# Kernel optimization log

Measured on AMD Instinct MI355X. Metric: run time of the kernel, lower is better.

## Reference

```python
import jax, jax.numpy as jnp
import numpy as np

B, IN_DIM, OUT_DIM, DEPTH = 8192, 4096, 2048, 9


def setup_inputs() -> dict:
    key = jax.random.key(0)
    k1, k2, k3, k4 = jax.random.split(key, 4)
    return {
        "x": jax.random.normal(k1, (B, IN_DIM), dtype=jnp.float32),
        "universal_weights": jax.random.normal(k2, (DEPTH, IN_DIM, OUT_DIM), dtype=jnp.float32),
        "classical_weights": jax.random.normal(k3, (IN_DIM, OUT_DIM), dtype=jnp.float32),
        "classical_biases": jax.random.normal(k4, (OUT_DIM,), dtype=jnp.float32),
    }


def _universal_probs(universal_weights, out_dim, in_dim):
    # Angles: original indexes universal_weights[depth, j, c] with j over output
    # dims and c in {0,1,2} (consciousness/intelligence/wisdom gates per depth).
    # Build the scan sequence in (depth, gate) order: shape (3*DEPTH, O).
    A = jnp.transpose(universal_weights[:, :out_dim, :3], (0, 2, 1)).reshape(-1, out_dim)
    # Initial state ones/sqrt(n), one independent state per output channel: (O, n)
    s0 = jnp.full((out_dim, in_dim), 1.0 / np.sqrt(in_dim), dtype=universal_weights.dtype)

    def step(s, ang):
        # Circulant tridiagonal rotation: diag=cos, super(+wrap)=-sin, sub(+wrap)=sin
        c = jnp.cos(ang)[:, None]
        sn = jnp.sin(ang)[:, None]
        s_next = c * s - sn * jnp.roll(s, -1, axis=1) + sn * jnp.roll(s, 1, axis=1)
        return s_next, None

    s, _ = jax.lax.scan(step, s0, A)
    # probability = |state[0]|^2 ; state is real so this is just the square
    return s[:, 0] ** 2  # (O,)


def reference(x, universal_weights, classical_weights, classical_biases):
    out_dim = classical_weights.shape[1]
    in_dim = x.shape[1]
    classical = x @ classical_weights + classical_biases  # (B, O)
    # Universal output is independent of the batch row (loop over i is dead code)
    probs = _universal_probs(universal_weights, out_dim, in_dim)  # (O,)
    return jnp.tanh(classical + probs[None, :])
```

## Files before the change

### kernel.cpp

```cpp
#include <hip/hip_runtime.h>
#include <cstdint>
#include <cstddef>

#define MM 8192
#define KK 4096
#define NN 2048
#define DEPTH_N 9

typedef __attribute__((ext_vector_type(8))) short bf16x8;
typedef __attribute__((ext_vector_type(16))) float f32x16;

static_assert(sizeof(bf16x8) == 16, "bf16x8 must be 16B");
static_assert(sizeof(f32x16) == 64, "f32x16 must be 64B");

typedef const __attribute__((address_space(1))) uint32_t* gptr_t;
typedef __attribute__((address_space(3))) uint32_t* lptr_t;

__device__ __forceinline__ void load_lds16(const void* g, void* l) {
  __builtin_amdgcn_global_load_lds((gptr_t)g, (lptr_t)l, 16, 0, 0);
}

union FragU {
  uint32_t u[4];
  bf16x8 v;
};

__device__ __forceinline__ void split4(float4 v, uint32_t& h01, uint32_t& h23,
                                       uint32_t& l01, uint32_t& l23) {
  uint32_t ux = __float_as_uint(v.x), uy = __float_as_uint(v.y);
  uint32_t uz = __float_as_uint(v.z), uw = __float_as_uint(v.w);
  h01 = __builtin_amdgcn_perm(uy, ux, 0x07060302u);
  h23 = __builtin_amdgcn_perm(uw, uz, 0x07060302u);
  float rx = v.x - __uint_as_float(ux & 0xFFFF0000u);
  float ry = v.y - __uint_as_float(uy & 0xFFFF0000u);
  float rz = v.z - __uint_as_float(uz & 0xFFFF0000u);
  float rw = v.w - __uint_as_float(uw & 0xFFFF0000u);
  l01 = __builtin_amdgcn_perm(__float_as_uint(ry), __float_as_uint(rx), 0x07060302u);
  l23 = __builtin_amdgcn_perm(__float_as_uint(rw), __float_as_uint(rz), 0x07060302u);
}

__global__ __launch_bounds__(256) void prep_bt_kernel(
    const float* __restrict__ W,
    uint16_t* __restrict__ btHi,
    uint16_t* __restrict__ btLo) {
  __shared__ float tile[64][65];
  const int k0 = blockIdx.x * 64;
  const int n0 = blockIdx.y * 64;
  const int c4 = (threadIdx.x & 15) * 4;
  const int r16 = threadIdx.x >> 4;
#pragma unroll
  for (int p = 0; p < 4; ++p) {
    int r = p * 16 + r16;
    float4 v = *(const float4*)(W + (size_t)(k0 + r) * NN + n0 + c4);
    tile[r][c4 + 0] = v.x;
    tile[r][c4 + 1] = v.y;
    tile[r][c4 + 2] = v.z;
    tile[r][c4 + 3] = v.w;
  }
  __syncthreads();
#pragma unroll
  for (int p = 0; p < 4; ++p) {
    int n = p * 16 + r16;
    ushort4 h, l;
    float f0 = tile[c4 + 0][n];
    float f1 = tile[c4 + 1][n];
    float f2 = tile[c4 + 2][n];
    float f3 = tile[c4 + 3][n];
    uint32_t u0 = __float_as_uint(f0), u1 = __float_as_uint(f1);
    uint32_t u2 = __float_as_uint(f2), u3 = __float_as_uint(f3);
    h.x = (uint16_t)(u0 >> 16);
    h.y = (uint16_t)(u1 >> 16);
    h.z = (uint16_t)(u2 >> 16);
    h.w = (uint16_t)(u3 >> 16);
    float r0 = f0 - __uint_as_float(u0 & 0xFFFF0000u);
    float r1 = f1 - __uint_as_float(u1 & 0xFFFF0000u);
    float r2 = f2 - __uint_as_float(u2 & 0xFFFF0000u);
    float r3 = f3 - __uint_as_float(u3 & 0xFFFF0000u);
    l.x = (uint16_t)(__float_as_uint(r0) >> 16);
    l.y = (uint16_t)(__float_as_uint(r1) >> 16);
    l.z = (uint16_t)(__float_as_uint(r2) >> 16);
    l.w = (uint16_t)(__float_as_uint(r3) >> 16);
    size_t off = (size_t)(n0 + n) * KK + k0 + c4;
    *(ushort4*)(btHi + off) = h;
    *(ushort4*)(btLo + off) = l;
  }
}

__global__ __launch_bounds__(256) void prep_x_kernel(
    const float* __restrict__ X,
    uint16_t* __restrict__ xHi,
    uint16_t* __restrict__ xLo) {
  size_t i = ((size_t)blockIdx.x * 256 + threadIdx.x) * 8;
  float4 v0 = *(const float4*)(X + i);
  float4 v1 = *(const float4*)(X + i + 4);
  uint32_t h01, h23, l01, l23, h45, h67, l45, l67;
  split4(v0, h01, h23, l01, l23);
  split4(v1, h45, h67, l45, l67);
  uint4 h, l;
  h.x = h01; h.y = h23; h.z = h45; h.w = h67;
  l.x = l01; l.y = l23; l.z = l45; l.w = l67;
  *(uint4*)(xHi + i) = h;
  *(uint4*)(xLo + i) = l;
}

__global__ __launch_bounds__(256) void prep_bias_kernel(
    const float* __restrict__ uw,
    const float* __restrict__ cb,
    float* __restrict__ bias2) {
  int j = blockIdx.x * 256 + threadIdx.x;
  float p = 1.0f / (float)KK;
#pragma unroll
  for (int d = 0; d < DEPTH_N; ++d) {
    float4 v = *(const float4*)(uw + (size_t)d * KK * NN + (size_t)j * NN);
    float c0 = cosf(v.x), c1 = cosf(v.y), c2 = cosf(v.z);
    p *= (c0 * c0) * (c1 * c1) * (c2 * c2);
  }
  bias2[j] = cb[j] + p;
}

__global__ __launch_bounds__(256, 4) void unl_gemm_ps_kernel(
    const uint16_t* __restrict__ XHi,
    const uint16_t* __restrict__ XLo,
    const uint16_t* __restrict__ BtHi,
    const uint16_t* __restrict__ BtLo,
    const float* __restrict__ bias2,
    float* __restrict__ Out) {
  __shared__ __align__(16) uint8_t smem[32768];
  char* sAh = (char*)smem;
  char* sAl = (char*)smem + 8192;
  char* sBh = (char*)smem + 16384;
  char* sBl = (char*)smem + 24576;

  const int tid = threadIdx.x;
  const int lane = tid & 63;
  const int wq = __builtin_amdgcn_readfirstlane(tid >> 6);
  const int wM = wq >> 1;
  const int wN = wq & 1;
  const int lane31 = lane & 31;
  const int kh = lane >> 5;

  const int bidx = blockIdx.x;
  const int m0 = (bidx & 63) * 128;
  const int n0 = (bidx >> 6) * 128;

  const int bC = (lane & 3) ^ ((lane >> 3) & 3);
  const int bVoff = ((lane >> 2) * KK + bC * 8) * 2;
  const char* aBaseH = (const char*)(XHi + (size_t)(m0 + wq * 32) * KK) + bVoff;
  const char* aBaseL = (const char*)(XLo + (size_t)(m0 + wq * 32) * KK) + bVoff;
  const char* bBaseH = (const char*)(BtHi + (size_t)(n0 + wq * 32) * KK) + bVoff;
  const char* bBaseL = (const char*)(BtLo + (size_t)(n0 + wq * 32) * KK) + bVoff;

  int aOffB[2][2], bOffB[2][2];
#pragma unroll
  for (int mt = 0; mt < 2; ++mt) {
    int row = wM * 64 + mt * 32 + lane31;
#pragma unroll
    for (int s = 0; s < 2; ++s)
      aOffB[mt][s] = row * 64 + (((2 * s + kh) ^ ((row >> 1) & 3)) * 16);
  }
#pragma unroll
  for (int nt = 0; nt < 2; ++nt) {
    int row = wN * 64 + nt * 32 + lane31;
#pragma unroll
    for (int s = 0; s < 2; ++s)
      bOffB[nt][s] = row * 64 + (((2 * s + kh) ^ ((row >> 1) & 3)) * 16);
  }

  f32x16 acc[2][2];
#pragma unroll
  for (int mt = 0; mt < 2; ++mt)
#pragma unroll
    for (int nt = 0; nt < 2; ++nt)
#pragma unroll
      for (int r = 0; r < 16; ++r) acc[mt][nt][r] = 0.0f;

  for (int kt = 0; kt < KK; kt += 32) {
    __syncthreads();
#pragma unroll
    for (int q = 0; q < 2; ++q) {
      load_lds16(aBaseH + (size_t)kt * 2 + (size_t)q * (16 * KK * 2),
                 sAh + (wq * 2 + q) * 1024);
      load_lds16(aBaseL + (size_t)kt * 2 + (size_t)q * (16 * KK * 2),
                 sAl + (wq * 2 + q) * 1024);
      load_lds16(bBaseH + (size_t)kt * 2 + (size_t)q * (16 * KK * 2),
                 sBh + (wq * 2 + q) * 1024);
      load_lds16(bBaseL + (size_t)kt * 2 + (size_t)q * (16 * KK * 2),
                 sBl + (wq * 2 + q) * 1024);
    }
    __syncthreads();

#pragma unroll
    for (int s = 0; s < 2; ++s) {
      bf16x8 ah[2], al[2], bh[2], bl[2];
#pragma unroll
      for (int mt = 0; mt < 2; ++mt) {
        ah[mt] = *(const bf16x8*)(sAh + aOffB[mt][s]);
        al[mt] = *(const bf16x8*)(sAl + aOffB[mt][s]);
      }
#pragma unroll
      for (int nt = 0; nt < 2; ++nt) {
        bh[nt] = *(const bf16x8*)(sBh + bOffB[nt][s]);
        bl[nt] = *(const bf16x8*)(sBl + bOffB[nt][s]);
      }
#pragma unroll
      for (int mt = 0; mt < 2; ++mt) {
#pragma unroll
        for (int nt = 0; nt < 2; ++nt) {
          acc[mt][nt] = __builtin_amdgcn_mfma_f32_32x32x16_bf16(ah[mt], bh[nt], acc[mt][nt], 0, 0, 0);
          acc[mt][nt] = __builtin_amdgcn_mfma_f32_32x32x16_bf16(ah[mt], bl[nt], acc[mt][nt], 0, 0, 0);
          acc[mt][nt] = __builtin_amdgcn_mfma_f32_32x32x16_bf16(al[mt], bh[nt], acc[mt][nt], 0, 0, 0);
        }
      }
    }
  }

#pragma unroll
  for (int nt = 0; nt < 2; ++nt) {
    int col = n0 + wN * 64 + nt * 32 + lane31;
    float b2 = bias2[col];
#pragma unroll
    for (int mt = 0; mt < 2; ++mt) {
#pragma unroll
      for (int r = 0; r < 16; ++r) {
        int rowl = (r & 3) + 8 * (r >> 2) + 4 * kh;
        int grow = m0 + wM * 64 + mt * 32 + rowl;
        float z = acc[mt][nt][r] + b2;
        z = fminf(fmaxf(z, -12.0f), 12.0f);
        float t = __expf(2.0f * z);
        Out[(size_t)grow * NN + col] = (t - 1.0f) / (t + 1.0f);
      }
    }
  }
}

__global__ __launch_bounds__(256, 4) void unl_gemm_kernel(
    const float* __restrict__ X,
    const uint16_t* __restrict__ BtHi,
    const uint16_t* __restrict__ BtLo,
    const float* __restrict__ bias2,
    float* __restrict__ Out) {
  __shared__ __align__(16) uint8_t smem[32768];
  char* sA = (char*)smem;
  char* sBh = (char*)smem + 16384;
  char* sBl = (char*)smem + 24576;

  const int tid = threadIdx.x;
  const int lane = tid & 63;
  const int wq = __builtin_amdgcn_readfirstlane(tid >> 6);
  const int wM = wq >> 1;
  const int wN = wq & 1;
  const int lane31 = lane & 31;
  const int kh = lane >> 5;

  const int bidx = blockIdx.x;
  const int m0 = (bidx & 63) * 128;
  const int n0 = (bidx >> 6) * 128;

  const int aC = (lane & 7) ^ (lane >> 3);
  const int aVoff = ((lane >> 3) * KK + aC * 4) * 4;
  const char* aBase = (const char*)(X + (size_t)(m0 + wq * 32) * KK) + aVoff;
  const int bC = (lane & 3) ^ ((lane >> 3) & 3);
  const int bVoff = ((lane >> 2) * KK + bC * 8) * 2;
  const char* bBaseH = (const char*)(BtHi + (size_t)(n0 + wq * 32) * KK) + bVoff;
  const char* bBaseL = (const char*)(BtLo + (size_t)(n0 + wq * 32) * KK) + bVoff;

  int aOffB[2][2];
#pragma unroll
  for (int mt = 0; mt < 2; ++mt) {
    int row = wM * 64 + mt * 32 + lane31;
#pragma unroll
    for (int s = 0; s < 2; ++s)
      aOffB[mt][s] = row * 128 + (((4 * s + 2 * kh) ^ (row & 7)) * 16);
  }
  int bOffB[2][2];
#pragma unroll
  for (int nt = 0; nt < 2; ++nt) {
    int row = wN * 64 + nt * 32 + lane31;
#pragma unroll
    for (int s = 0; s < 2; ++s)
      bOffB[nt][s] = row * 64 + (((2 * s + kh) ^ ((row >> 1) & 3)) * 16);
  }

  f32x16 acc[2][2];
#pragma unroll
  for (int mt = 0; mt < 2; ++mt)
#pragma unroll
    for (int nt = 0; nt < 2; ++nt)
#pragma unroll
      for (int r = 0; r < 16; ++r) acc[mt][nt][r] = 0.0f;

  for (int kt = 0; kt < KK; kt += 32) {
    __syncthreads();
#pragma unroll
    for (int q = 0; q < 4; ++q)
      load_lds16(aBase + (size_t)kt * 4 + (size_t)q * (8 * KK * 4),
                 sA + (wq * 4 + q) * 1024);
#pragma unroll
    for (int q = 0; q < 2; ++q) {
      load_lds16(bBaseH + (size_t)kt * 2 + (size_t)q * (16 * KK * 2),
                 sBh + (wq * 2 + q) * 1024);
      load_lds16(bBaseL + (size_t)kt * 2 + (size_t)q * (16 * KK * 2),
                 sBl + (wq * 2 + q) * 1024);
    }
    __syncthreads();

#pragma unroll
    for (int s = 0; s < 2; ++s) {
      bf16x8 ah[2], al[2], bh[2], bl[2];
#pragma unroll
      for (int mt = 0; mt < 2; ++mt) {
        float4 v0 = *(const float4*)(sA + aOffB[mt][s]);
        float4 v1 = *(const float4*)(sA + (aOffB[mt][s] ^ 16));
        FragU uh, ul;
        split4(v0, uh.u[0], uh.u[1], ul.u[0], ul.u[1]);
        split4(v1, uh.u[2], uh.u[3], ul.u[2], ul.u[3]);
        ah[mt] = uh.v;
        al[mt] = ul.v;
      }
#pragma unroll
      for (int nt = 0; nt < 2; ++nt) {
        bh[nt] = *(const bf16x8*)(sBh + bOffB[nt][s]);
        bl[nt] = *(const bf16x8*)(sBl + bOffB[nt][s]);
      }
#pragma unroll
      for (int mt = 0; mt < 2; ++mt) {
#pragma unroll
        for (int nt = 0; nt < 2; ++nt) {
          acc[mt][nt] = __builtin_amdgcn_mfma_f32_32x32x16_bf16(ah[mt], bh[nt], acc[mt][nt], 0, 0, 0);
          acc[mt][nt] = __builtin_amdgcn_mfma_f32_32x32x16_bf16(ah[mt], bl[nt], acc[mt][nt], 0, 0, 0);
          acc[mt][nt] = __builtin_amdgcn_mfma_f32_32x32x16_bf16(al[mt], bh[nt], acc[mt][nt], 0, 0, 0);
        }
      }
    }
  }

#pragma unroll
  for (int nt = 0; nt < 2; ++nt) {
    int col = n0 + wN * 64 + nt * 32 + lane31;
    float b2 = bias2[col];
#pragma unroll
    for (int mt = 0; mt < 2; ++mt) {
#pragma unroll
      for (int r = 0; r < 16; ++r) {
        int rowl = (r & 3) + 8 * (r >> 2) + 4 * kh;
        int grow = m0 + wM * 64 + mt * 32 + rowl;
        float z = acc[mt][nt][r] + b2;
        z = fminf(fmaxf(z, -12.0f), 12.0f);
        float t = __expf(2.0f * z);
        Out[(size_t)grow * NN + col] = (t - 1.0f) / (t + 1.0f);
      }
    }
  }
}

extern "C" void kernel_launch(void* const* d_in, const int* in_sizes, int n_in,
                              void* d_out, int out_size, void* d_ws, size_t ws_size,
                              hipStream_t stream) {
  const float* x = (const float*)d_in[0];
  const float* uw = (const float*)d_in[1];
  const float* cw = (const float*)d_in[2];
  const float* cb = (const float*)d_in[3];
  float* out = (float*)d_out;

  uint16_t* btHi = (uint16_t*)d_ws;
  uint16_t* btLo = btHi + (size_t)NN * KK;
  float* bias2 = (float*)(btLo + (size_t)NN * KK);
  uint16_t* xHi = (uint16_t*)(bias2 + NN);
  uint16_t* xLo = xHi + (size_t)MM * KK;

  const size_t need = (size_t)NN * KK * 4
                    + (size_t)NN * 4
                    + (size_t)MM * KK * 4;

  prep_bt_kernel<<<dim3(KK / 64, NN / 64), 256, 0, stream>>>(cw, btHi, btLo);
  prep_bias_kernel<<<dim3(NN / 256), 256, 0, stream>>>(uw, cb, bias2);

  if (ws_size >= need) {
    prep_x_kernel<<<dim3((MM * KK) / (256 * 8)), 256, 0, stream>>>(x, xHi, xLo);
    unl_gemm_ps_kernel<<<dim3((MM / 128) * (NN / 128)), 256, 0, stream>>>(
        xHi, xLo, btHi, btLo, bias2, out);
  } else {
    unl_gemm_kernel<<<dim3((MM / 128) * (NN / 128)), 256, 0, stream>>>(
        x, btHi, btLo, bias2, out);
  }
}
```

Baseline: 876.4 us.

## Replace split-bf16 GEMM with 256x256 tile, double-buffered three-pass pipeline

Replaces the 128x128 tile kernel with a 256x256 tile kernel using 512 threads and 128KB of dynamic LDS. Each K-slice gets double-buffered async global-to-LDS loads, controlled by vmcnt waits and raw barriers. The hi*hi, hi*lo and lo*hi products become three sequential passes over K (192 stages) rather than being interleaved per slice. It also adds a block swizzle for L2 locality, XOR-swizzled LDS layout, and setprio around the MFMA groups. In exchange it uses more LDS and registers per block and runs a single block wave on the 256-CU device.

```diff
diff --git a/kernel.cpp b/kernel.cpp
--- a/kernel.cpp
+++ b/kernel.cpp
@@ -118,100 +118,111 @@
   bias2[j] = cb[j] + p;
 }
 
-__global__ __launch_bounds__(256, 4) void unl_gemm_ps_kernel(
+__device__ __forceinline__ void stage_tile(
+    int g, char* smembase,
+    const char* pAh, const char* pAl, const char* pBh, const char* pBl,
+    uint32_t aSrcOff, uint32_t bSrcOff, uint32_t aLdsOff, uint32_t bLdsOff) {
+  const int pass = g >> 6;
+  const int kt = g & 63;
+  const char* pA = (pass == 2) ? pAl : pAh;
+  const char* pB = (pass == 1) ? pBl : pBh;
+  const uint32_t kOff = (uint32_t)kt * 128;
+  char* la = smembase + (size_t)((g & 1) * 65536) + aLdsOff;
+  char* lb = smembase + (size_t)((g & 1) * 65536 + 32768) + bLdsOff;
+#pragma unroll
+  for (int q = 0; q < 4; ++q) {
+    load_lds16(pA + (size_t)(aSrcOff + kOff) + (size_t)q * (8 * KK * 2), la + q * 1024);
+    load_lds16(pB + (size_t)(bSrcOff + kOff) + (size_t)q * (8 * KK * 2), lb + q * 1024);
+  }
+}
+
+__global__ __launch_bounds__(512, 2) void gemm256_kernel(
     const uint16_t* __restrict__ XHi,
     const uint16_t* __restrict__ XLo,
     const uint16_t* __restrict__ BtHi,
     const uint16_t* __restrict__ BtLo,
     const float* __restrict__ bias2,
     float* __restrict__ Out) {
-  __shared__ __align__(16) uint8_t smem[32768];
-  char* sAh = (char*)smem;
-  char* sAl = (char*)smem + 8192;
-  char* sBh = (char*)smem + 16384;
-  char* sBl = (char*)smem + 24576;
+  extern __shared__ __align__(16) char smem[];
 
   const int tid = threadIdx.x;
   const int lane = tid & 63;
   const int wq = __builtin_amdgcn_readfirstlane(tid >> 6);
-  const int wM = wq >> 1;
-  const int wN = wq & 1;
+  const int wM = wq >> 2;
+  const int wN = wq & 3;
   const int lane31 = lane & 31;
   const int kh = lane >> 5;
 
-  const int bidx = blockIdx.x;
-  const int m0 = (bidx & 63) * 128;
-  const int n0 = (bidx >> 6) * 128;
-
-  const int bC = (lane & 3) ^ ((lane >> 3) & 3);
-  const int bVoff = ((lane >> 2) * KK + bC * 8) * 2;
-  const char* aBaseH = (const char*)(XHi + (size_t)(m0 + wq * 32) * KK) + bVoff;
-  const char* aBaseL = (const char*)(XLo + (size_t)(m0 + wq * 32) * KK) + bVoff;
-  const char* bBaseH = (const char*)(BtHi + (size_t)(n0 + wq * 32) * KK) + bVoff;
-  const char* bBaseL = (const char*)(BtLo + (size_t)(n0 + wq * 32) * KK) + bVoff;
-
-  int aOffB[2][2], bOffB[2][2];
-#pragma unroll
-  for (int mt = 0; mt < 2; ++mt) {
-    int row = wM * 64 + mt * 32 + lane31;
-#pragma unroll
-    for (int s = 0; s < 2; ++s)
-      aOffB[mt][s] = row * 64 + (((2 * s + kh) ^ ((row >> 1) & 3)) * 16);
-  }
-#pragma unroll
-  for (int nt = 0; nt < 2; ++nt) {
-    int row = wN * 64 + nt * 32 + lane31;
-#pragma unroll
-    for (int s = 0; s < 2; ++s)
-      bOffB[nt][s] = row * 64 + (((2 * s + kh) ^ ((row >> 1) & 3)) * 16);
-  }
-
-  f32x16 acc[2][2];
-#pragma unroll
-  for (int mt = 0; mt < 2; ++mt)
+  const int bid = blockIdx.x;
+  const int swz = (bid & 7) * 32 + (bid >> 3);
+  const int m0 = (swz >> 3) * 256;
+  const int n0 = (swz & 7) * 256;
+
+  const uint32_t swzBlk = (uint32_t)(((lane & 7) ^ (lane >> 3)) * 16);
+  const uint32_t aSrcOff =
+      (uint32_t)(m0 + wM * 128 + wN * 32 + (lane >> 3)) * (KK * 2) + swzBlk;
+  const uint32_t bSrcOff =
+      (uint32_t)(n0 + wN * 64 + wM * 32 + (lane >> 3)) * (KK * 2) + swzBlk;
+  const uint32_t aLdsOff = (uint32_t)(wM * 128 + wN * 32) * 128;
+  const uint32_t bLdsOff = (uint32_t)(wN * 64 + wM * 32) * 128;
+
+  uint32_t aRowB[4], bRowB[2], xk[4];
+#pragma unroll
+  for (int mt = 0; mt < 4; ++mt)
+    aRowB[mt] = (uint32_t)(wM * 128 + mt * 32 + lane31) * 128;
+#pragma unroll
+  for (int nt = 0; nt < 2; ++nt)
+    bRowB[nt] = (uint32_t)(wN * 64 + nt * 32 + lane31) * 128;
+#pragma unroll
+  for (int ks = 0; ks < 4; ++ks)
+    xk[ks] = (uint32_t)(((2 * ks + kh) ^ (lane31 & 7)) * 16);
+
+  f32x16 acc[4][2];
+#pragma unroll
+  for (int mt = 0; mt < 4; ++mt)
 #pragma unroll
     for (int nt = 0; nt < 2; ++nt)
 #pragma unroll
       for (int r = 0; r < 16; ++r) acc[mt][nt][r] = 0.0f;
 
-  for (int kt = 0; kt < KK; kt += 32) {
-    __syncthreads();
-#pragma unroll
-    for (int q = 0; q < 2; ++q) {
-      load_lds16(aBaseH + (size_t)kt * 2 + (size_t)q * (16 * KK * 2),
-                 sAh + (wq * 2 + q) * 1024);
-      load_lds16(aBaseL + (size_t)kt * 2 + (size_t)q * (16 * KK * 2),
-                 sAl + (wq * 2 + q) * 1024);
-      load_lds16(bBaseH + (size_t)kt * 2 + (size_t)q * (16 * KK * 2),
-                 sBh + (wq * 2 + q) * 1024);
-      load_lds16(bBaseL + (size_t)kt * 2 + (size_t)q * (16 * KK * 2),
-                 sBl + (wq * 2 + q) * 1024);
-    }
-    __syncthreads();
-
-#pragma unroll
-    for (int s = 0; s < 2; ++s) {
-      bf16x8 ah[2], al[2], bh[2], bl[2];
-#pragma unroll
-      for (int mt = 0; mt < 2; ++mt) {
-        ah[mt] = *(const bf16x8*)(sAh + aOffB[mt][s]);
-        al[mt] = *(const bf16x8*)(sAl + aOffB[mt][s]);
-      }
-#pragma unroll
-      for (int nt = 0; nt < 2; ++nt) {
-        bh[nt] = *(const bf16x8*)(sBh + bOffB[nt][s]);
-        bl[nt] = *(const bf16x8*)(sBl + bOffB[nt][s]);
-      }
-#pragma unroll
-      for (int mt = 0; mt < 2; ++mt) {
-#pragma unroll
-        for (int nt = 0; nt < 2; ++nt) {
-          acc[mt][nt] = __builtin_amdgcn_mfma_f32_32x32x16_bf16(ah[mt], bh[nt], acc[mt][nt], 0, 0, 0);
-          acc[mt][nt] = __builtin_amdgcn_mfma_f32_32x32x16_bf16(ah[mt], bl[nt], acc[mt][nt], 0, 0, 0);
-          acc[mt][nt] = __builtin_amdgcn_mfma_f32_32x32x16_bf16(al[mt], bh[nt], acc[mt][nt], 0, 0, 0);
-        }
-      }
-    }
+  const char* pAh = (const char*)XHi;
+  const char* pAl = (const char*)XLo;
+  const char* pBh = (const char*)BtHi;
+  const char* pBl = (const char*)BtLo;
+
+  stage_tile(0, smem, pAh, pAl, pBh, pBl, aSrcOff, bSrcOff, aLdsOff, bLdsOff);
+
+  for (int g = 0; g < 192; ++g) {
+    if (g + 1 < 192) {
+      stage_tile(g + 1, smem, pAh, pAl, pBh, pBl, aSrcOff, bSrcOff, aLdsOff, bLdsOff);
+      asm volatile("s_waitcnt vmcnt(8)" ::: "memory");
+    } else {
+      asm volatile("s_waitcnt vmcnt(0)" ::: "memory");
+    }
+    __builtin_amdgcn_s_barrier();
+    __builtin_amdgcn_sched_barrier(0);
+
+    const char* bufA = smem + (size_t)((g & 1) * 65536);
+    const char* bufB = bufA + 32768;
+#pragma unroll
+    for (int ks = 0; ks < 4; ++ks) {
+      bf16x8 af[4], bfr[2];
+#pragma unroll
+      for (int mt = 0; mt < 4; ++mt)
+        af[mt] = *(const bf16x8*)(bufA + aRowB[mt] + xk[ks]);
+#pragma unroll
+      for (int nt = 0; nt < 2; ++nt)
+        bfr[nt] = *(const bf16x8*)(bufB + bRowB[nt] + xk[ks]);
+      __builtin_amdgcn_s_setprio(1);
+#pragma unroll
+      for (int mt = 0; mt < 4; ++mt)
+#pragma unroll
+        for (int nt = 0; nt < 2; ++nt)
+          acc[mt][nt] = __builtin_amdgcn_mfma_f32_32x32x16_bf16(
+              af[mt], bfr[nt], acc[mt][nt], 0, 0, 0);
+      __builtin_amdgcn_s_setprio(0);
+    }
+    __builtin_amdgcn_s_barrier();
   }
 
 #pragma unroll
@@ -219,11 +230,11 @@
     int col = n0 + wN * 64 + nt * 32 + lane31;
     float b2 = bias2[col];
 #pragma unroll
-    for (int mt = 0; mt < 2; ++mt) {
+    for (int mt = 0; mt < 4; ++mt) {
 #pragma unroll
       for (int r = 0; r < 16; ++r) {
         int rowl = (r & 3) + 8 * (r >> 2) + 4 * kh;
-        int grow = m0 + wM * 64 + mt * 32 + rowl;
+        int grow = m0 + wM * 128 + mt * 32 + rowl;
         float z = acc[mt][nt][r] + b2;
         z = fminf(fmaxf(z, -12.0f), 12.0f);
         float t = __expf(2.0f * z);
@@ -377,7 +388,13 @@
 
   if (ws_size >= need) {
     prep_x_kernel<<<dim3((MM * KK) / (256 * 8)), 256, 0, stream>>>(x, xHi, xLo);
-    unl_gemm_ps_kernel<<<dim3((MM / 128) * (NN / 128)), 256, 0, stream>>>(
+    static bool attr_set = false;
+    if (!attr_set) {
+      hipFuncSetAttribute((const void*)gemm256_kernel,
+                          hipFuncAttributeMaxDynamicSharedMemorySize, 131072);
+      attr_set = true;
+    }
+    gemm256_kernel<<<dim3((MM / 256) * (NN / 256)), 512, 131072, stream>>>(
         xHi, xLo, btHi, btLo, bias2, out);
   } else {
     unl_gemm_kernel<<<dim3((MM / 128) * (NN / 128)), 256, 0, stream>>>(
```

Measured after the change: 844.8 us. 1.04x faster.
